# Optimization experiments

Hardware: AMD Instinct MI355X
Metric: run time of the kernel (lower is better)

The kernel has to match this reference:

```python
import jax, jax.numpy as jnp
import numpy as np

B, C1, C2, H, W, NH = 16, 256, 256, 64, 64, 8
C = C2 // 2          # hidden dim of retention blocks (c2*e)
HD = C // NH         # head dim
EPS = 1e-5           # torch BatchNorm2d / LayerNorm default eps


def _ln(x, g, b):
    mu = jnp.mean(x, -1, keepdims=True)
    var = jnp.mean((x - mu) ** 2, -1, keepdims=True)
    return (x - mu) * jax.lax.rsqrt(var + EPS) * g + b


def _bn_silu(y, g, b, m, v):
    # inference-mode BatchNorm2d (running stats) + SiLU, channels axis=1
    y = (y - m[:, None, None]) * jax.lax.rsqrt(v + EPS)[:, None, None] * g[:, None, None] + b[:, None, None]
    return jax.nn.silu(y)


def _decay1d(L, dec):
    # RelPos2d.generate_1d_decay: exp(decay_n * |i-j|), shape (NH, L, L)
    idx = jnp.arange(L)
    m = jnp.abs(idx[:, None] - idx[None, :]).astype(jnp.float32)
    return jnp.exp(dec[:, None, None] * m)


def setup_inputs() -> dict:
    key = jax.random.key(0)
    ks = jax.random.split(key, 8)
    s = 0.02
    return {
        'x': jax.random.normal(ks[0], (B, C1, H, W), jnp.float32),
        'cv1_w': jax.random.normal(ks[1], (2 * C, C1), jnp.float32) * s,
        'bn1_g': jnp.ones((2 * C,)), 'bn1_b': jnp.zeros((2 * C,)),
        'bn1_m': jnp.zeros((2 * C,)), 'bn1_v': jnp.ones((2 * C,)),
        'cv2_w': jax.random.normal(ks[2], (C2, 3 * C), jnp.float32) * s,
        'bn2_g': jnp.ones((C2,)), 'bn2_b': jnp.zeros((C2,)),
        'bn2_m': jnp.zeros((C2,)), 'bn2_v': jnp.ones((C2,)),
        'ln1_g': jnp.ones((C,)), 'ln1_b': jnp.zeros((C,)),
        'qkv_w': jax.random.normal(ks[3], (3 * C, C), jnp.float32) * s,
        'qkv_b': jnp.zeros((3 * C,)),
        'proj_w': jax.random.normal(ks[4], (C, C), jnp.float32) * s,
        'proj_b': jnp.zeros((C,)),
        'gamma': jnp.ones((C,)),
        'ln2_g': jnp.ones((C,)), 'ln2_b': jnp.zeros((C,)),
        'ffn_w1': jax.random.normal(ks[5], (2 * C, C), jnp.float32) * s,
        'ffn_b1': jnp.zeros((2 * C,)),
        'ffn_w2': jax.random.normal(ks[6], (C, 2 * C), jnp.float32) * s,
        'ffn_b2': jnp.zeros((C,)),
    }


def reference(x, cv1_w, bn1_g, bn1_b, bn1_m, bn1_v, cv2_w, bn2_g, bn2_b, bn2_m, bn2_v,
              ln1_g, ln1_b, qkv_w, qkv_b, proj_w, proj_b, gamma,
              ln2_g, ln2_b, ffn_w1, ffn_b1, ffn_w2, ffn_b2):
    # RelPos2d: decay per head, initial_value=2, heads_range=4; mode='chunk' -> 1D decays
    dec = jnp.log(1.0 - 2.0 ** (-2.0 - 4.0 * jnp.arange(NH, dtype=jnp.float32) / NH))
    decay_h = _decay1d(H, dec)  # (NH, H, H)
    decay_w = _decay1d(W, dec)  # (NH, W, W)

    # cv1: 1x1 conv + BN + SiLU, then chunk into two halves of C channels
    y = _bn_silu(jnp.einsum('bchw,oc->bohw', x, cv1_w), bn1_g, bn1_b, bn1_m, bn1_v)
    y1, y2 = y[:, :C], y[:, C:]

    # RetBlock on channels-last feature map
    f = jnp.transpose(y2, (0, 2, 3, 1))  # (B,H,W,C)
    res = f
    fn = _ln(f, ln1_g, ln1_b)
    qkv = fn @ qkv_w.T + qkv_b
    q, k, v = jnp.split(qkv, 3, axis=-1)

    def heads(t):
        return jnp.transpose(t.reshape(B, H, W, NH, HD), (0, 3, 1, 2, 4))  # (B,NH,H,W,HD)

    q, k, v = heads(q), heads(k), heads(v)

    # axial retention: row attention with exponential row-decay
    qk_h = jnp.einsum('bnhwc,bnHwc->bnhHw', q, k) * decay_h[None, :, :, :, None]
    out_h = jnp.einsum('bnhHw,bnHwc->bnhwc', qk_h, v)
    # column attention with exponential column-decay
    qk_w = jnp.einsum('bnhwc,bnhWc->bnhwW', q, k) * decay_w[None, :, None, :, :]
    out_w = jnp.einsum('bnhwW,bnhWc->bnhwc', qk_w, v)
    out = 0.5 * (out_h + out_w)
    out = jnp.transpose(out, (0, 2, 3, 1, 4)).reshape(B, H, W, C)

    f = res + (out @ proj_w.T + proj_b) * gamma
    res2 = f
    fn2 = _ln(f, ln2_g, ln2_b)
    h1 = jax.nn.gelu(fn2 @ ffn_w1.T + ffn_b1, approximate=False)
    f = res2 + (h1 @ ffn_w2.T + ffn_b2)

    f = jnp.transpose(f, (0, 3, 1, 2))  # back to (B,C,H,W)
    cat = jnp.concatenate([y1, y2, f], axis=1)  # (B,3C,H,W)
    return _bn_silu(jnp.einsum('bchw,oc->bohw', cat, cv2_w), bn2_g, bn2_b, bn2_m, bn2_v)
```

## Files before the change

### kernel.cpp

```cpp
#include <hip/hip_runtime.h>
#include <math.h>

#define LEPS 1e-5f
static constexpr int NPOS = 65536;

typedef __attribute__((ext_vector_type(8))) short short8;
typedef __attribute__((ext_vector_type(4))) float floatx4;

__device__ __forceinline__ ushort f2bf(float f) {
    unsigned int u = __float_as_uint(f);
    u += 0x7FFF + ((u >> 16) & 1);
    return (ushort)(u >> 16);
}
__device__ __forceinline__ float bfu(ushort h) {
    return __uint_as_float((unsigned int)h << 16);
}
__device__ __forceinline__ float bfl(unsigned int u) {
    return __uint_as_float(u << 16);
}
__device__ __forceinline__ float bfh(unsigned int u) {
    return __uint_as_float(u & 0xffff0000u);
}

typedef __attribute__((address_space(1))) const unsigned int gu32_t;
typedef __attribute__((address_space(3))) unsigned int lu32_t;
__device__ __forceinline__ void gld16(const ushort* g, ushort* l) {
    __builtin_amdgcn_global_load_lds((gu32_t*)g, (lu32_t*)l, 16, 0, 0);
}

struct WcvtArgs { const float* src[6]; ushort* dst[6]; int n[6]; };
__global__ __launch_bounds__(256)
void wcvt_k(WcvtArgs a)
{
    const int seg = blockIdx.y;
    const float* s = a.src[seg];
    ushort* d = a.dst[seg];
    const int n = a.n[seg];
    for (int i = blockIdx.x * 256 + threadIdx.x; i < n; i += gridDim.x * 256)
        d[i] = f2bf(s[i]);
}

__global__ __launch_bounds__(256)
void bnprep_k(const float* g1, const float* b1, const float* m1, const float* v1,
              const float* g2, const float* b2, const float* m2, const float* v2,
              float* s1, float* h1, float* s2, float* h2)
{
    const int i = threadIdx.x;
    if (blockIdx.x == 0) {
        const float s = g1[i] * rsqrtf(v1[i] + LEPS);
        s1[i] = s; h1[i] = b1[i] - m1[i] * s;
    } else {
        const float s = g2[i] * rsqrtf(v2[i] + LEPS);
        s2[i] = s; h2[i] = b2[i] - m2[i] * s;
    }
}

__global__ __launch_bounds__(256)
void tr_k(const float* __restrict__ x, ushort* __restrict__ xT)
{
    __shared__ float tile[64][65];
    const int t = threadIdx.x;
    const int bi = blockIdx.x;
    const int hwt = bi & 63, ct = (bi >> 6) & 3, b = bi >> 8;
    const int p0 = b * 4096 + hwt * 64, c0 = ct * 64;
    const float* src = x + ((size_t)(b * 256 + c0) << 12) + hwt * 64;
#pragma unroll
    for (int i = 0; i < 16; i++) {
        int cc = (t >> 6) + i * 4;
        tile[cc][t & 63] = src[((size_t)cc << 12) + (t & 63)];
    }
    __syncthreads();
    const int c2 = (t & 31) * 2;
    const int pr = t >> 5;
#pragma unroll
    for (int i = 0; i < 8; i++) {
        int pp = pr + i * 8;
        unsigned int u = (unsigned int)f2bf(tile[c2][pp])
                       | ((unsigned int)f2bf(tile[c2 + 1][pp]) << 16);
        *(unsigned int*)&xT[(size_t)(p0 + pp) * 256 + c0 + c2] = u;
    }
}

template<int KDIM, int ARS, int AMODE, int EPI, int LN>
__global__ __launch_bounds__(256)
void gemm_k(const ushort* __restrict__ A0, const ushort* __restrict__ A1,
            const ushort* __restrict__ Wm, const float* __restrict__ bias,
            const float* __restrict__ q0, const float* __restrict__ q1,
            const ushort* __restrict__ resh,
            const float* __restrict__ lng, const float* __restrict__ lnb,
            ushort* __restrict__ lnout, void* __restrict__ outv, int ors)
{
    constexpr int NT = KDIM / 64;
    __shared__ __align__(16) ushort smem[24576];
    const int t = threadIdx.x;
    const int p0 = blockIdx.x * 64;
    const int o0 = blockIdx.y * 128;
    const int lane = t & 63, wv = t >> 6;
    const int wn = wv * 32;
    const int ln15 = lane & 15, quad = lane >> 4;
    const int dl_row = lane >> 3;
    const int dl_sch = (lane & 7) ^ dl_row;
    const int c_off0 = ((quad) ^ (ln15 & 7)) * 8;
    const int c_off1 = ((4 + quad) ^ (ln15 & 7)) * 8;
    floatx4 acc[4][2] = {};

    const int a3row = t >> 2, a3q = t & 3;
    uint4 ra[2], rb4[2];

    auto stageA = [&](int k0, int bc) {
#pragma unroll
        for (int i = 0; i < 2; i++) {
            const int r0 = wv * 16 + i * 8;
            const int row = r0 + dl_row;
            const ushort* src;
            if (AMODE == 2) {
                if (k0 < 256) src = A0 + (size_t)(p0 + row) * 256 + k0 + dl_sch * 8;
                else          src = A1 + (size_t)(p0 + row) * 128 + (k0 - 256) + dl_sch * 8;
            } else {
                src = A0 + (size_t)(p0 + row) * ARS + k0 + dl_sch * 8;
            }
            gld16(src, &smem[bc * 4096 + r0 * 64]);
        }
    };
    auto stageB = [&](int k0, int bc) {
#pragma unroll
        for (int i = 0; i < 4; i++) {
            const int r0 = wv * 32 + i * 8;
            gld16(Wm + (size_t)(o0 + r0 + dl_row) * KDIM + k0 + dl_sch * 8,
                  &smem[8192 + bc * 8192 + r0 * 64]);
        }
    };
    auto loadA3 = [&](int k0) {
        const ushort* s1 = A0 + (size_t)(p0 + a3row) * 128 + k0 + a3q * 16;
        const ushort* s2 = A1 + (size_t)(p0 + a3row) * 128 + k0 + a3q * 16;
#pragma unroll
        for (int i = 0; i < 2; i++) { ra[i] = ((const uint4*)s1)[i]; rb4[i] = ((const uint4*)s2)[i]; }
    };
    auto writeA3 = [&](int bc) {
#pragma unroll
        for (int i = 0; i < 2; i++) {
            const unsigned int* ap = (const unsigned int*)&ra[i];
            const unsigned int* bp = (const unsigned int*)&rb4[i];
            uint4 w; unsigned int* wp = (unsigned int*)&w;
#pragma unroll
            for (int j = 0; j < 4; j++)
                wp[j] = (unsigned int)f2bf(0.5f * (bfl(ap[j]) + bfl(bp[j])))
                      | ((unsigned int)f2bf(0.5f * (bfh(ap[j]) + bfh(bp[j]))) << 16);
            const int pch = (a3q * 2 + i) ^ (a3row & 7);
            *(uint4*)&smem[bc * 4096 + a3row * 64 + pch * 8] = w;
        }
    };
    auto compute = [&](int bc) {
#pragma unroll
        for (int kh = 0; kh < 2; kh++) {
            const int co = kh ? c_off1 : c_off0;
            short8 a[4], b[2];
#pragma unroll
            for (int i = 0; i < 4; i++)
                a[i] = *(const short8*)&smem[bc * 4096 + (i * 16 + ln15) * 64 + co];
#pragma unroll
            for (int j = 0; j < 2; j++)
                b[j] = *(const short8*)&smem[8192 + bc * 8192 + (wn + j * 16 + ln15) * 64 + co];
#pragma unroll
            for (int i = 0; i < 4; i++)
#pragma unroll
                for (int j = 0; j < 2; j++)
                    acc[i][j] = __builtin_amdgcn_mfma_f32_16x16x32_bf16(
                        a[i], b[j], acc[i][j], 0, 0, 0);
        }
    };

    if (AMODE == 3) {
        loadA3(0);
        stageB(0, 0);
#pragma unroll
        for (int tt = 0; tt < NT; ++tt) {
            const int cur = tt & 1;
            writeA3(cur);
            if (tt + 1 < NT) {
                loadA3((tt + 1) * 64);
                stageB((tt + 1) * 64, cur ^ 1);
                asm volatile("s_waitcnt vmcnt(8) lgkmcnt(0)" ::: "memory");
            } else {
                asm volatile("s_waitcnt vmcnt(0) lgkmcnt(0)" ::: "memory");
            }
            __builtin_amdgcn_s_barrier();
            __builtin_amdgcn_sched_barrier(0);
            compute(cur);
            __builtin_amdgcn_sched_barrier(0);
            __builtin_amdgcn_s_barrier();
        }
    } else {
        stageA(0, 0); stageB(0, 0);
#pragma unroll
        for (int tt = 0; tt < NT; ++tt) {
            const int cur = tt & 1;
            if (tt + 1 < NT) {
                stageA((tt + 1) * 64, cur ^ 1);
                stageB((tt + 1) * 64, cur ^ 1);
                asm volatile("s_waitcnt vmcnt(6)" ::: "memory");
            } else {
                asm volatile("s_waitcnt vmcnt(0)" ::: "memory");
            }
            __builtin_amdgcn_s_barrier();
            __builtin_amdgcn_sched_barrier(0);
            compute(cur);
            __builtin_amdgcn_sched_barrier(0);
            __builtin_amdgcn_s_barrier();
        }
    }

    if (EPI == 2) {
        float* cb = (float*)smem;
        float* ob = (float*)outv + (((size_t)(p0 >> 12) * 256) << 12);
        const int hw0 = p0 & 4095;
#pragma unroll
        for (int chunk = 0; chunk < 2; chunk++) {
            __syncthreads();
            if ((wv >> 1) == chunk) {
#pragma unroll
                for (int i = 0; i < 4; i++)
#pragma unroll
                for (int j = 0; j < 2; j++) {
                    const int chl = (wv & 1) * 32 + j * 16 + ln15;
                    const int o = o0 + chunk * 64 + chl;
                    const float sc = q0[o], sh = q1[o];
#pragma unroll
                    for (int r = 0; r < 4; r++) {
                        const int pos = i * 16 + quad * 4 + r;
                        float v = acc[i][j][r] * sc + sh;
                        v = v / (1.f + __expf(-v));
                        cb[chl * 72 + pos] = v;
                    }
                }
            }
            __syncthreads();
#pragma unroll
            for (int it = 0; it < 4; it++) {
                const int flat = it * 256 + t;
                const int ch = flat >> 4, posq = (flat & 15) * 4;
                const int o = o0 + chunk * 64 + ch;
                float4 v4 = *(const float4*)&cb[ch * 72 + posq];
                *(float4*)&ob[((size_t)o << 12) + hw0 + posq] = v4;
            }
        }
        return;
    }

    const bool lnact = LN && (EPI != 1 || o0 == 128);
    ushort (*lt)[136] = (ushort (*)[136])smem;
#pragma unroll
    for (int i = 0; i < 4; i++) {
#pragma unroll
        for (int r = 0; r < 4; r++) {
            const int lr = i * 16 + quad * 4 + r;
            const int p = p0 + lr;
#pragma unroll
            for (int j = 0; j < 2; j++) {
                const int ol = wn + j * 16 + ln15;
                const int o = o0 + ol;
                float v = acc[i][j][r];
                if (EPI == 0) {
                    v += bias[o];
                } else if (EPI == 1) {
                    v = v * q0[o] + q1[o];
                    v = v / (1.f + __expf(-v));
                } else if (EPI == 4) {
                    v = bfu(resh[(size_t)p * 256 + 128 + o]) + (v + bias[o]) * q0[o];
                }
                lt[lr][ol] = f2bf(v);
            }
        }
    }
    __syncthreads();
    {
        ushort* o16 = (ushort*)outv;
#pragma unroll
        for (int it = 0; it < 4; it++) {
            const int flat = it * 256 + t;
            const int row = flat >> 4, ch = (flat & 15) * 8;
            *(uint4*)&o16[(size_t)(p0 + row) * (size_t)ors + o0 + ch] =
                *(const uint4*)&lt[row][ch];
        }
    }

    if (lnact && t < 128) {
        const int rrow = t >> 1, rhalf = t & 1;
        const ushort* rp = &lt[rrow][rhalf * 64];
        float s = 0.f, s2 = 0.f;
#pragma unroll
        for (int i = 0; i < 8; i++) {
            const uint4 u = *(const uint4*)(rp + i * 8);
            const unsigned int ww[4] = {u.x, u.y, u.z, u.w};
#pragma unroll
            for (int j = 0; j < 4; j++) {
                const float a = bfl(ww[j]), c = bfh(ww[j]);
                s += a + c; s2 += a * a + c * c;
            }
        }
        s += __shfl_xor(s, 1); s2 += __shfl_xor(s2, 1);
        const float mu = s * (1.f / 128.f);
        const float rn = rsqrtf(s2 * (1.f / 128.f) - mu * mu + LEPS);
        ushort* op = lnout + (size_t)(p0 + rrow) * 128 + rhalf * 64;
#pragma unroll
        for (int i = 0; i < 8; i++) {
            const uint4 u = *(const uint4*)(rp + i * 8);
            const unsigned int ww[4] = {u.x, u.y, u.z, u.w};
            uint4 wout;
            unsigned int* wo = (unsigned int*)&wout;
#pragma unroll
            for (int j = 0; j < 4; j++) {
                const int ch = rhalf * 64 + i * 8 + j * 2;
                const float2 gg = *(const float2*)(lng + ch);
                const float2 bb = *(const float2*)(lnb + ch);
                const float a = (bfl(ww[j]) - mu) * rn * gg.x + bb.x;
                const float c = (bfh(ww[j]) - mu) * rn * gg.y + bb.y;
                wo[j] = (unsigned int)f2bf(a) | ((unsigned int)f2bf(c) << 16);
            }
            *(uint4*)(op + i * 8) = wout;
        }
    }
}

__global__ __launch_bounds__(256)
void ffn_k(const ushort* __restrict__ fn2, const ushort* __restrict__ w1,
           const float* __restrict__ b1, const ushort* __restrict__ w2,
           const float* __restrict__ b2, ushort* __restrict__ f)
{
    __shared__ __align__(16) ushort smem[40960];
    const int t = threadIdx.x;
    const int p0 = blockIdx.x * 64;
    const int lane = t & 63, wv = t >> 6;
    const int ln15 = lane & 15, quad = lane >> 4;
    const int dl_row = lane >> 3;
    const int dl_sch = (lane & 7) ^ dl_row;
    const int dl4_row = lane >> 4;
    const int dl4_c   = lane & 15;
    const int c_off0 = ((quad) ^ (ln15 & 7)) * 8;
    const int c_off1 = ((4 + quad) ^ (ln15 & 7)) * 8;

    float bb1[4], bb2[2];
#pragma unroll
    for (int j = 0; j < 4; j++) bb1[j] = b1[wv * 64 + j * 16 + ln15];
#pragma unroll
    for (int j = 0; j < 2; j++) bb2[j] = b2[wv * 32 + j * 16 + ln15];

#pragma unroll
    for (int i = 0; i < 4; i++) {
        const int r0 = wv * 16 + i * 4;
        const int row = r0 + dl4_row;
        const int sch = dl4_c ^ (row & 7);
        gld16(fn2 + (size_t)(p0 + row) * 128 + sch * 8, &smem[r0 * 128]);
    }
#pragma unroll
    for (int i = 0; i < 16; i++) {
        const int r0 = wv * 64 + i * 4;
        const int row = r0 + dl4_row;
        const int sch = dl4_c ^ (row & 7);
        gld16(w1 + (size_t)row * 128 + sch * 8, &smem[8192 + r0 * 128]);
    }
    asm volatile("s_waitcnt vmcnt(0)" ::: "memory");
    __builtin_amdgcn_s_barrier();
    __builtin_amdgcn_sched_barrier(0);

    floatx4 acc1[4][4] = {};
#pragma unroll
    for (int kk = 0; kk < 4; kk++) {
        const int co = ((kk * 4 + quad) ^ (ln15 & 7)) * 8;
        short8 a[4], b[4];
#pragma unroll
        for (int i = 0; i < 4; i++)
            a[i] = *(const short8*)&smem[(i * 16 + ln15) * 128 + co];
#pragma unroll
        for (int j = 0; j < 4; j++)
            b[j] = *(const short8*)&smem[8192 + (wv * 64 + j * 16 + ln15) * 128 + co];
#pragma unroll
        for (int i = 0; i < 4; i++)
#pragma unroll
            for (int j = 0; j < 4; j++)
                acc1[i][j] = __builtin_amdgcn_mfma_f32_16x16x32_bf16(
                    a[i], b[j], acc1[i][j], 0, 0, 0);
    }
    __builtin_amdgcn_s_barrier();
    __builtin_amdgcn_sched_barrier(0);

#pragma unroll
    for (int i = 0; i < 4; i++) {
        const int r0 = wv * 32 + i * 8;
        gld16(w2 + (size_t)(r0 + dl_row) * 256 + dl_sch * 8,
              &smem[16896 + r0 * 64]);
    }
    {
        ushort (*H1w)[264] = (ushort (*)[264])smem;
#pragma unroll
        for (int i = 0; i < 4; i++)
#pragma unroll
        for (int j = 0; j < 4; j++)
#pragma unroll
        for (int r = 0; r < 4; r++) {
            float v = acc1[i][j][r] + bb1[j];
            v = 0.5f * v * (1.f + erff(v * 0.70710678118654752f));
            H1w[i * 16 + quad * 4 + r][wv * 64 + j * 16 + ln15] = f2bf(v);
        }
    }
    asm volatile("s_waitcnt lgkmcnt(0)" ::: "memory");
    __builtin_amdgcn_s_barrier();
    __builtin_amdgcn_sched_barrier(0);

    ushort (*H1)[264] = (ushort (*)[264])smem;
    floatx4 acc2[4][2] = {};
#pragma unroll
    for (int t4 = 0; t4 < 4; ++t4) {
        const int cur = t4 & 1;
        if (t4 + 1 < 4) {
#pragma unroll
            for (int i = 0; i < 4; i++) {
                const int r0 = wv * 32 + i * 8;
                gld16(w2 + (size_t)(r0 + dl_row) * 256 + (t4 + 1) * 64 + dl_sch * 8,
                      &smem[16896 + (cur ^ 1) * 8192 + r0 * 64]);
            }
            asm volatile("s_waitcnt vmcnt(4)" ::: "memory");
        } else {
#pragma unroll
            for (int i = 0; i < 4; i++) {
                const int r0 = wv * 16 + i * 4;
                gld16(f + (size_t)(p0 + r0 + (lane >> 4)) * 128 + (lane & 15) * 8,
                      &smem[16896 + (cur ^ 1) * 8192 + r0 * 128]);
            }
            asm volatile("s_waitcnt vmcnt(4)" ::: "memory");
        }
        __builtin_amdgcn_s_barrier();
        __builtin_amdgcn_sched_barrier(0);
#pragma unroll
        for (int kh = 0; kh < 2; kh++) {
            const int co = kh ? c_off1 : c_off0;
            short8 a[4], b[2];
#pragma unroll
            for (int i = 0; i < 4; i++)
                a[i] = *(const short8*)&H1[i * 16 + ln15][t4 * 64 + kh * 32 + quad * 8];
#pragma unroll
            for (int j = 0; j < 2; j++)
                b[j] = *(const short8*)&smem[16896 + cur * 8192
                                             + (wv * 32 + j * 16 + ln15) * 64 + co];
#pragma unroll
            for (int i = 0; i < 4; i++)
#pragma unroll
                for (int j = 0; j < 2; j++)
                    acc2[i][j] = __builtin_amdgcn_mfma_f32_16x16x32_bf16(
                        a[i], b[j], acc2[i][j], 0, 0, 0);
        }
        __builtin_amdgcn_sched_barrier(0);
        __builtin_amdgcn_s_barrier();
    }
    asm volatile("s_waitcnt vmcnt(0)" ::: "memory");
    __builtin_amdgcn_s_barrier();

    ushort* Ft = &smem[16896];
    {
#pragma unroll
        for (int i = 0; i < 4; i++)
#pragma unroll
        for (int r = 0; r < 4; r++) {
            const int pos = i * 16 + quad * 4 + r;
#pragma unroll
            for (int j = 0; j < 2; j++) {
                const int ch = wv * 32 + j * 16 + ln15;
                const int idx = pos * 128 + ch;
                Ft[idx] = f2bf(bfu(Ft[idx]) + acc2[i][j][r] + bb2[j]);
            }
        }
    }
    __syncthreads();
#pragma unroll
    for (int it = 0; it < 4; it++) {
        const int flat = it * 256 + t;
        const int row = flat >> 4, ch = (flat & 15) * 8;
        *(uint4*)&f[(size_t)(p0 + row) * 128 + ch] = *(const uint4*)&Ft[row * 128 + ch];
    }
}

__global__ __launch_bounds__(256)
void attn_k(const ushort* __restrict__ qkv, ushort* __restrict__ oh,
            ushort* __restrict__ ow)
{
    __shared__ ushort VtS[4][16 * 72];
    __shared__ ushort SbS[4][64 * 72];
    __shared__ float dpow[128];
    const int t = threadIdx.x, wv = t >> 6, lane = t & 63;
    const int ln15 = lane & 15, quad = lane >> 4;
    const int dirH = (blockIdx.y == 0);
    ushort* outb = dirH ? oh : ow;
    const int blk = blockIdx.x;
    const int lg = blk & 15, n = (blk >> 4) & 7, b = blk >> 7;
    if (t < 128) {
        const float dec = logf(1.f - exp2f(-2.f - 0.5f * (float)n));
        int d = t - 63; if (d < 0) d = -d;
        dpow[t] = __expf(dec * (float)d);
    }
    const int fixed = lg * 4 + wv;
    const int stride = dirH ? 64 : 1;
    const size_t base = (size_t)b * 4096 + (dirH ? fixed : fixed * 64);
    const size_t cbase = base * 384 + n * 16;

    {
        const ushort* vp = qkv + cbase + (size_t)lane * stride * 384 + 256;
        const uint4 va = *(const uint4*)vp, vb = *(const uint4*)(vp + 8);
        ushort* vt = VtS[wv] + lane;
        const unsigned int w[8] = { va.x, va.y, va.z, va.w, vb.x, vb.y, vb.z, vb.w };
#pragma unroll
        for (int d = 0; d < 8; d++) {
            vt[(2 * d) * 72]     = (ushort)(w[d] & 0xffff);
            vt[(2 * d + 1) * 72] = (ushort)(w[d] >> 16);
        }
    }
    short8 qa[4], kb[4];
    {
        const short8 z = {0, 0, 0, 0, 0, 0, 0, 0};
#pragma unroll
        for (int mt = 0; mt < 4; mt++) {
            const int i = mt * 16 + ln15;
            if (quad < 2) {
                const ushort* qp = qkv + cbase + (size_t)i * stride * 384 + quad * 8;
                qa[mt] = *(const short8*)qp;
                kb[mt] = *(const short8*)(qp + 128);
            } else { qa[mt] = z; kb[mt] = z; }
        }
    }
    __syncthreads();

#pragma unroll
    for (int mt = 0; mt < 4; mt++) {
#pragma unroll
        for (int nt = 0; nt < 4; nt++) {
            floatx4 c = {0.f, 0.f, 0.f, 0.f};
            c = __builtin_amdgcn_mfma_f32_16x16x32_bf16(qa[mt], kb[nt], c, 0, 0, 0);
            const int i0 = mt * 16 + quad * 4;
            const int jl = nt * 16 + ln15;
            const float* lut = dpow + (i0 - jl + 63);
            ushort* sb = SbS[wv] + i0 * 72 + jl;
#pragma unroll
            for (int r = 0; r < 4; r++)
                sb[r * 72] = f2bf(c[r] * lut[r]);
        }
    }
    __syncthreads();

    short8 av[2];
#pragma unroll
    for (int c = 0; c < 2; c++)
        av[c] = *(const short8*)&VtS[wv][ln15 * 72 + c * 32 + quad * 8];
    floatx4 o[4] = {};
#pragma unroll
    for (int nt4 = 0; nt4 < 4; nt4++) {
#pragma unroll
        for (int c = 0; c < 2; c++) {
            const short8 bs = *(const short8*)
                &SbS[wv][(nt4 * 16 + ln15) * 72 + c * 32 + quad * 8];
            o[nt4] = __builtin_amdgcn_mfma_f32_16x16x32_bf16(av[c], bs, o[nt4], 0, 0, 0);
        }
    }
#pragma unroll
    for (int nt4 = 0; nt4 < 4; nt4++) {
        const int i = nt4 * 16 + ln15;
        ushort* op = outb + (base + (size_t)i * stride) * 128 + n * 16 + quad * 4;
        uint2 w;
        w.x = (unsigned int)f2bf(o[nt4][0]) | ((unsigned int)f2bf(o[nt4][1]) << 16);
        w.y = (unsigned int)f2bf(o[nt4][2]) | ((unsigned int)f2bf(o[nt4][3]) << 16);
        *(uint2*)op = w;
    }
}

extern "C" void kernel_launch(void* const* d_in, const int* in_sizes, int n_in,
                              void* d_out, int out_size, void* d_ws, size_t ws_size,
                              hipStream_t stream)
{
    const float* x      = (const float*)d_in[0];
    const float* cv1_w  = (const float*)d_in[1];
    const float* bn1_g  = (const float*)d_in[2];
    const float* bn1_b  = (const float*)d_in[3];
    const float* bn1_m  = (const float*)d_in[4];
    const float* bn1_v  = (const float*)d_in[5];
    const float* cv2_w  = (const float*)d_in[6];
    const float* bn2_g  = (const float*)d_in[7];
    const float* bn2_b  = (const float*)d_in[8];
    const float* bn2_m  = (const float*)d_in[9];
    const float* bn2_v  = (const float*)d_in[10];
    const float* ln1_g  = (const float*)d_in[11];
    const float* ln1_b  = (const float*)d_in[12];
    const float* qkv_w  = (const float*)d_in[13];
    const float* qkv_b  = (const float*)d_in[14];
    const float* proj_w = (const float*)d_in[15];
    const float* proj_b = (const float*)d_in[16];
    const float* gamma  = (const float*)d_in[17];
    const float* ln2_g  = (const float*)d_in[18];
    const float* ln2_b  = (const float*)d_in[19];
    const float* ffn_w1 = (const float*)d_in[20];
    const float* ffn_b1 = (const float*)d_in[21];
    const float* ffn_w2 = (const float*)d_in[22];
    const float* ffn_b2 = (const float*)d_in[23];

    ushort* W = (ushort*)d_ws;
    ushort* y    = W;
    ushort* f    = y    + (size_t)NPOS * 256;
    ushort* tmp  = f    + (size_t)NPOS * 128;
    ushort* owb  = tmp  + (size_t)NPOS * 128;
    ushort* qkvb = owb  + (size_t)NPOS * 128;
    ushort* xT   = qkvb + (size_t)NPOS * 384;
    ushort* wc1  = xT   + (size_t)NPOS * 256;
    ushort* wqkv = wc1  + 65536;
    ushort* wpr  = wqkv + 49152;
    ushort* ww1  = wpr  + 16384;
    ushort* ww2  = ww1  + 32768;
    ushort* wc2  = ww2  + 32768;
    float*  bns1 = (float*)(wc2 + 98304);
    float*  bnb1 = bns1 + 256;
    float*  bns2 = bnb1 + 256;
    float*  bnb2 = bns2 + 256;
    float*  out  = (float*)d_out;

    WcvtArgs wa;
    wa.src[0] = cv1_w;  wa.dst[0] = wc1;  wa.n[0] = 65536;
    wa.src[1] = qkv_w;  wa.dst[1] = wqkv; wa.n[1] = 49152;
    wa.src[2] = proj_w; wa.dst[2] = wpr;  wa.n[2] = 16384;
    wa.src[3] = ffn_w1; wa.dst[3] = ww1;  wa.n[3] = 32768;
    wa.src[4] = ffn_w2; wa.dst[4] = ww2;  wa.n[4] = 32768;
    wa.src[5] = cv2_w;  wa.dst[5] = wc2;  wa.n[5] = 98304;
    wcvt_k<<<dim3(96, 6), 256, 0, stream>>>(wa);
    bnprep_k<<<2, 256, 0, stream>>>(bn1_g, bn1_b, bn1_m, bn1_v,
                                    bn2_g, bn2_b, bn2_m, bn2_v,
                                    bns1, bnb1, bns2, bnb2);
    tr_k<<<4096, 256, 0, stream>>>(x, xT);

    gemm_k<256, 256, 0, 1, 1><<<dim3(1024, 2), 256, 0, stream>>>(
        xT, nullptr, wc1, nullptr, bns1, bnb1, nullptr, ln1_g, ln1_b, tmp, y, 256);
    gemm_k<128, 128, 0, 0, 0><<<dim3(1024, 3), 256, 0, stream>>>(
        tmp, nullptr, wqkv, qkv_b, nullptr, nullptr, nullptr, nullptr, nullptr,
        nullptr, qkvb, 384);
    attn_k<<<dim3(2048, 2), 256, 0, stream>>>(qkvb, tmp, owb);
    gemm_k<128, 128, 3, 4, 1><<<dim3(1024, 1), 256, 0, stream>>>(
        tmp, owb, wpr, proj_b, gamma, nullptr, y, ln2_g, ln2_b, tmp, f, 128);
    ffn_k<<<1024, 256, 0, stream>>>(tmp, ww1, ffn_b1, ww2, ffn_b2, f);
    gemm_k<384, 0, 2, 2, 0><<<dim3(1024, 2), 256, 0, stream>>>(
        y, f, wc2, nullptr, bns2, bnb2, nullptr, nullptr, nullptr, nullptr, out, 0);
}
```

Measured before the change: 334.2 us.

## Fuse projection, residual, LayerNorm2 and FFN into one kernel

Merges the proj GEMM (with the out_h/out_w averaging, bias, gamma and residual) and the FFN kernel into a single pf_k kernel. The post-projection residual stays in registers and LayerNorm2 is computed in shared memory, so the f and fn2 intermediates no longer round-trip through global memory, and one launch is removed. To fit shared memory, the FFN first GEMM is restructured to stream w1 in 64-row chunks. This may reduce overlap or occupancy compared with the previous two-kernel arrangement.

```diff
diff --git a/kernel.cpp b/kernel.cpp
--- a/kernel.cpp
+++ b/kernel.cpp
@@ -86,7 +86,6 @@
 void gemm_k(const ushort* __restrict__ A0, const ushort* __restrict__ A1,
             const ushort* __restrict__ Wm, const float* __restrict__ bias,
             const float* __restrict__ q0, const float* __restrict__ q1,
-            const ushort* __restrict__ resh,
             const float* __restrict__ lng, const float* __restrict__ lnb,
             ushort* __restrict__ lnout, void* __restrict__ outv, int ors)
 {
@@ -104,9 +103,6 @@
     const int c_off1 = ((4 + quad) ^ (ln15 & 7)) * 8;
     floatx4 acc[4][2] = {};
 
-    const int a3row = t >> 2, a3q = t & 3;
-    uint4 ra[2], rb4[2];
-
     auto stageA = [&](int k0, int bc) {
 #pragma unroll
         for (int i = 0; i < 2; i++) {
@@ -130,26 +126,6 @@
                   &smem[8192 + bc * 8192 + r0 * 64]);
         }
     };
-    auto loadA3 = [&](int k0) {
-        const ushort* s1 = A0 + (size_t)(p0 + a3row) * 128 + k0 + a3q * 16;
-        const ushort* s2 = A1 + (size_t)(p0 + a3row) * 128 + k0 + a3q * 16;
-#pragma unroll
-        for (int i = 0; i < 2; i++) { ra[i] = ((const uint4*)s1)[i]; rb4[i] = ((const uint4*)s2)[i]; }
-    };
-    auto writeA3 = [&](int bc) {
-#pragma unroll
-        for (int i = 0; i < 2; i++) {
-            const unsigned int* ap = (const unsigned int*)&ra[i];
-            const unsigned int* bp = (const unsigned int*)&rb4[i];
-            uint4 w; unsigned int* wp = (unsigned int*)&w;
-#pragma unroll
-            for (int j = 0; j < 4; j++)
-                wp[j] = (unsigned int)f2bf(0.5f * (bfl(ap[j]) + bfl(bp[j])))
-                      | ((unsigned int)f2bf(0.5f * (bfh(ap[j]) + bfh(bp[j]))) << 16);
-            const int pch = (a3q * 2 + i) ^ (a3row & 7);
-            *(uint4*)&smem[bc * 4096 + a3row * 64 + pch * 8] = w;
-        }
-    };
     auto compute = [&](int bc) {
 #pragma unroll
         for (int kh = 0; kh < 2; kh++) {
@@ -170,44 +146,22 @@
         }
     };
 
-    if (AMODE == 3) {
-        loadA3(0);
-        stageB(0, 0);
-#pragma unroll
-        for (int tt = 0; tt < NT; ++tt) {
-            const int cur = tt & 1;
-            writeA3(cur);
-            if (tt + 1 < NT) {
-                loadA3((tt + 1) * 64);
-                stageB((tt + 1) * 64, cur ^ 1);
-                asm volatile("s_waitcnt vmcnt(8) lgkmcnt(0)" ::: "memory");
-            } else {
-                asm volatile("s_waitcnt vmcnt(0) lgkmcnt(0)" ::: "memory");
-            }
-            __builtin_amdgcn_s_barrier();
-            __builtin_amdgcn_sched_barrier(0);
-            compute(cur);
-            __builtin_amdgcn_sched_barrier(0);
-            __builtin_amdgcn_s_barrier();
-        }
-    } else {
-        stageA(0, 0); stageB(0, 0);
-#pragma unroll
-        for (int tt = 0; tt < NT; ++tt) {
-            const int cur = tt & 1;
-            if (tt + 1 < NT) {
-                stageA((tt + 1) * 64, cur ^ 1);
-                stageB((tt + 1) * 64, cur ^ 1);
-                asm volatile("s_waitcnt vmcnt(6)" ::: "memory");
-            } else {
-                asm volatile("s_waitcnt vmcnt(0)" ::: "memory");
-            }
-            __builtin_amdgcn_s_barrier();
-            __builtin_amdgcn_sched_barrier(0);
-            compute(cur);
-            __builtin_amdgcn_sched_barrier(0);
-            __builtin_amdgcn_s_barrier();
-        }
+    stageA(0, 0); stageB(0, 0);
+#pragma unroll
+    for (int tt = 0; tt < NT; ++tt) {
+        const int cur = tt & 1;
+        if (tt + 1 < NT) {
+            stageA((tt + 1) * 64, cur ^ 1);
+            stageB((tt + 1) * 64, cur ^ 1);
+            asm volatile("s_waitcnt vmcnt(6)" ::: "memory");
+        } else {
+            asm volatile("s_waitcnt vmcnt(0)" ::: "memory");
+        }
+        __builtin_amdgcn_s_barrier();
+        __builtin_amdgcn_sched_barrier(0);
+        compute(cur);
+        __builtin_amdgcn_sched_barrier(0);
+        __builtin_amdgcn_s_barrier();
     }
 
     if (EPI == 2) {
@@ -254,7 +208,6 @@
 #pragma unroll
         for (int r = 0; r < 4; r++) {
             const int lr = i * 16 + quad * 4 + r;
-            const int p = p0 + lr;
 #pragma unroll
             for (int j = 0; j < 2; j++) {
                 const int ol = wn + j * 16 + ln15;
@@ -262,11 +215,9 @@
                 float v = acc[i][j][r];
                 if (EPI == 0) {
                     v += bias[o];
-                } else if (EPI == 1) {
+                } else {
                     v = v * q0[o] + q1[o];
                     v = v / (1.f + __expf(-v));
-                } else if (EPI == 4) {
-                    v = bfu(resh[(size_t)p * 256 + 128 + o]) + (v + bias[o]) * q0[o];
                 }
                 lt[lr][ol] = f2bf(v);
             }
@@ -323,15 +274,20 @@
 }
 
 __global__ __launch_bounds__(256)
-void ffn_k(const ushort* __restrict__ fn2, const ushort* __restrict__ w1,
-           const float* __restrict__ b1, const ushort* __restrict__ w2,
-           const float* __restrict__ b2, ushort* __restrict__ f)
+void pf_k(const ushort* __restrict__ oh, const ushort* __restrict__ ow,
+          const ushort* __restrict__ wpr, const float* __restrict__ pb,
+          const float* __restrict__ gamma, const ushort* __restrict__ resh,
+          const float* __restrict__ lng, const float* __restrict__ lnb,
+          const ushort* __restrict__ w1, const float* __restrict__ b1,
+          const ushort* __restrict__ w2, const float* __restrict__ b2,
+          ushort* __restrict__ f)
 {
-    __shared__ __align__(16) ushort smem[40960];
+    __shared__ __align__(16) ushort smem[33280];
     const int t = threadIdx.x;
     const int p0 = blockIdx.x * 64;
     const int lane = t & 63, wv = t >> 6;
     const int ln15 = lane & 15, quad = lane >> 4;
+    const int wn = wv * 32;
     const int dl_row = lane >> 3;
     const int dl_sch = (lane & 7) ^ dl_row;
     const int dl4_row = lane >> 4;
@@ -339,95 +295,201 @@
     const int c_off0 = ((quad) ^ (ln15 & 7)) * 8;
     const int c_off1 = ((4 + quad) ^ (ln15 & 7)) * 8;
 
-    float bb1[4], bb2[2];
-#pragma unroll
-    for (int j = 0; j < 4; j++) bb1[j] = b1[wv * 64 + j * 16 + ln15];
-#pragma unroll
-    for (int j = 0; j < 2; j++) bb2[j] = b2[wv * 32 + j * 16 + ln15];
-
+    const int a3row = t >> 2, a3q = t & 3;
+    uint4 ra[2], rb4[2];
+    auto loadA3 = [&](int k0) {
+        const ushort* s1 = oh + (size_t)(p0 + a3row) * 128 + k0 + a3q * 16;
+        const ushort* s2 = ow + (size_t)(p0 + a3row) * 128 + k0 + a3q * 16;
+#pragma unroll
+        for (int i = 0; i < 2; i++) { ra[i] = ((const uint4*)s1)[i]; rb4[i] = ((const uint4*)s2)[i]; }
+    };
+    auto writeA3 = [&](int bc) {
+#pragma unroll
+        for (int i = 0; i < 2; i++) {
+            const unsigned int* ap = (const unsigned int*)&ra[i];
+            const unsigned int* bp = (const unsigned int*)&rb4[i];
+            uint4 w; unsigned int* wp = (unsigned int*)&w;
+#pragma unroll
+            for (int j = 0; j < 4; j++)
+                wp[j] = (unsigned int)f2bf(0.5f * (bfl(ap[j]) + bfl(bp[j])))
+                      | ((unsigned int)f2bf(0.5f * (bfh(ap[j]) + bfh(bp[j]))) << 16);
+            const int pch = (a3q * 2 + i) ^ (a3row & 7);
+            *(uint4*)&smem[bc * 4096 + a3row * 64 + pch * 8] = w;
+        }
+    };
+    floatx4 accP[4][2] = {};
+
+    loadA3(0);
+#pragma unroll
+    for (int i = 0; i < 8; i++) {
+        const int r0 = wv * 32 + i * 4;
+        const int row = r0 + dl4_row;
+        gld16(wpr + (size_t)row * 128 + (dl4_c ^ (row & 7)) * 8,
+              &smem[8192 + r0 * 128]);
+    }
+#pragma unroll
+    for (int tt = 0; tt < 2; ++tt) {
+        const int cur = tt & 1;
+        writeA3(cur);
+        if (tt == 0) {
+            loadA3(64);
+            asm volatile("s_waitcnt vmcnt(8) lgkmcnt(0)" ::: "memory");
+        } else {
+            asm volatile("s_waitcnt vmcnt(0) lgkmcnt(0)" ::: "memory");
+        }
+        __builtin_amdgcn_s_barrier();
+        __builtin_amdgcn_sched_barrier(0);
+#pragma unroll
+        for (int kh = 0; kh < 2; kh++) {
+            const int coA = kh ? c_off1 : c_off0;
+            const int coB = ((tt * 8 + kh * 4 + quad) ^ (ln15 & 7)) * 8;
+            short8 a[4], b[2];
+#pragma unroll
+            for (int i = 0; i < 4; i++)
+                a[i] = *(const short8*)&smem[cur * 4096 + (i * 16 + ln15) * 64 + coA];
+#pragma unroll
+            for (int j = 0; j < 2; j++)
+                b[j] = *(const short8*)&smem[8192 + (wn + j * 16 + ln15) * 128 + coB];
+#pragma unroll
+            for (int i = 0; i < 4; i++)
+#pragma unroll
+                for (int j = 0; j < 2; j++)
+                    accP[i][j] = __builtin_amdgcn_mfma_f32_16x16x32_bf16(
+                        a[i], b[j], accP[i][j], 0, 0, 0);
+        }
+        __builtin_amdgcn_sched_barrier(0);
+        __builtin_amdgcn_s_barrier();
+    }
+
+    float fp[4][2][4];
+    ushort (*lt)[136] = (ushort (*)[136])&smem[8192];
+#pragma unroll
+    for (int i = 0; i < 4; i++)
+#pragma unroll
+    for (int r = 0; r < 4; r++) {
+        const int lr = i * 16 + quad * 4 + r;
+        const int p = p0 + lr;
+#pragma unroll
+        for (int j = 0; j < 2; j++) {
+            const int o = wn + j * 16 + ln15;
+            float v = bfu(resh[(size_t)p * 256 + 128 + o]) + (accP[i][j][r] + pb[o]) * gamma[o];
+            fp[i][j][r] = v;
+            lt[lr][o] = f2bf(v);
+        }
+    }
 #pragma unroll
     for (int i = 0; i < 4; i++) {
         const int r0 = wv * 16 + i * 4;
         const int row = r0 + dl4_row;
-        const int sch = dl4_c ^ (row & 7);
-        gld16(fn2 + (size_t)(p0 + row) * 128 + sch * 8, &smem[r0 * 128]);
-    }
-#pragma unroll
-    for (int i = 0; i < 16; i++) {
-        const int r0 = wv * 64 + i * 4;
-        const int row = r0 + dl4_row;
-        const int sch = dl4_c ^ (row & 7);
-        gld16(w1 + (size_t)row * 128 + sch * 8, &smem[8192 + r0 * 128]);
-    }
-    asm volatile("s_waitcnt vmcnt(0)" ::: "memory");
-    __builtin_amdgcn_s_barrier();
-    __builtin_amdgcn_sched_barrier(0);
-
-    floatx4 acc1[4][4] = {};
-#pragma unroll
-    for (int kk = 0; kk < 4; kk++) {
-        const int co = ((kk * 4 + quad) ^ (ln15 & 7)) * 8;
-        short8 a[4], b[4];
-#pragma unroll
-        for (int i = 0; i < 4; i++)
-            a[i] = *(const short8*)&smem[(i * 16 + ln15) * 128 + co];
-#pragma unroll
-        for (int j = 0; j < 4; j++)
-            b[j] = *(const short8*)&smem[8192 + (wv * 64 + j * 16 + ln15) * 128 + co];
-#pragma unroll
-        for (int i = 0; i < 4; i++)
-#pragma unroll
-            for (int j = 0; j < 4; j++)
-                acc1[i][j] = __builtin_amdgcn_mfma_f32_16x16x32_bf16(
-                    a[i], b[j], acc1[i][j], 0, 0, 0);
-    }
-    __builtin_amdgcn_s_barrier();
-    __builtin_amdgcn_sched_barrier(0);
-
-#pragma unroll
-    for (int i = 0; i < 4; i++) {
-        const int r0 = wv * 32 + i * 8;
-        gld16(w2 + (size_t)(r0 + dl_row) * 256 + dl_sch * 8,
-              &smem[16896 + r0 * 64]);
-    }
-    {
-        ushort (*H1w)[264] = (ushort (*)[264])smem;
-#pragma unroll
-        for (int i = 0; i < 4; i++)
-#pragma unroll
-        for (int j = 0; j < 4; j++)
-#pragma unroll
-        for (int r = 0; r < 4; r++) {
-            float v = acc1[i][j][r] + bb1[j];
-            v = 0.5f * v * (1.f + erff(v * 0.70710678118654752f));
-            H1w[i * 16 + quad * 4 + r][wv * 64 + j * 16 + ln15] = f2bf(v);
+        gld16(w1 + (size_t)row * 128 + (dl4_c ^ (row & 7)) * 8,
+              &smem[25088 + r0 * 128]);
+    }
+    __syncthreads();
+    if (t < 128) {
+        const int rrow = t >> 1, rhalf = t & 1;
+        const ushort* rp = &lt[rrow][rhalf * 64];
+        float s = 0.f, s2 = 0.f;
+#pragma unroll
+        for (int i = 0; i < 8; i++) {
+            const uint4 u = *(const uint4*)(rp + i * 8);
+            const unsigned int ww[4] = {u.x, u.y, u.z, u.w};
+#pragma unroll
+            for (int j = 0; j < 4; j++) {
+                const float a = bfl(ww[j]), c = bfh(ww[j]);
+                s += a + c; s2 += a * a + c * c;
+            }
+        }
+        s += __shfl_xor(s, 1); s2 += __shfl_xor(s2, 1);
+        const float mu = s * (1.f / 128.f);
+        const float rn = rsqrtf(s2 * (1.f / 128.f) - mu * mu + LEPS);
+#pragma unroll
+        for (int i = 0; i < 8; i++) {
+            const uint4 u = *(const uint4*)(rp + i * 8);
+            const unsigned int ww[4] = {u.x, u.y, u.z, u.w};
+            uint4 wout;
+            unsigned int* wo = (unsigned int*)&wout;
+#pragma unroll
+            for (int j = 0; j < 4; j++) {
+                const int ch = rhalf * 64 + i * 8 + j * 2;
+                const float2 gg = *(const float2*)(lng + ch);
+                const float2 bb = *(const float2*)(lnb + ch);
+                const float a = (bfl(ww[j]) - mu) * rn * gg.x + bb.x;
+                const float c = (bfh(ww[j]) - mu) * rn * gg.y + bb.y;
+                wo[j] = (unsigned int)f2bf(a) | ((unsigned int)f2bf(c) << 16);
+            }
+            const int c16 = (rhalf * 8 + i) ^ (rrow & 7);
+            *(uint4*)&smem[rrow * 128 + c16 * 8] = wout;
         }
     }
     asm volatile("s_waitcnt lgkmcnt(0)" ::: "memory");
     __builtin_amdgcn_s_barrier();
     __builtin_amdgcn_sched_barrier(0);
 
-    ushort (*H1)[264] = (ushort (*)[264])smem;
+    ushort* H1 = &smem[8192];
+    float bb2[2];
+#pragma unroll
+    for (int j = 0; j < 2; j++) bb2[j] = b2[wn + j * 16 + ln15];
+#pragma unroll
+    for (int q = 0; q < 4; q++) {
+        asm volatile("s_waitcnt vmcnt(0)" ::: "memory");
+        __builtin_amdgcn_s_barrier();
+        __builtin_amdgcn_sched_barrier(0);
+        const float bq = b1[q * 64 + wv * 16 + ln15];
+        floatx4 a1[4] = {};
+#pragma unroll
+        for (int kk = 0; kk < 4; kk++) {
+            const int co = ((kk * 4 + quad) ^ (ln15 & 7)) * 8;
+            short8 bfr = *(const short8*)&smem[25088 + (wv * 16 + ln15) * 128 + co];
+#pragma unroll
+            for (int i = 0; i < 4; i++) {
+                short8 afr = *(const short8*)&smem[(i * 16 + ln15) * 128 + co];
+                a1[i] = __builtin_amdgcn_mfma_f32_16x16x32_bf16(afr, bfr, a1[i], 0, 0, 0);
+            }
+        }
+#pragma unroll
+        for (int i = 0; i < 4; i++)
+#pragma unroll
+        for (int r = 0; r < 4; r++) {
+            float v = a1[i][r] + bq;
+            v = 0.5f * v * (1.f + erff(v * 0.70710678118654752f));
+            H1[(i * 16 + quad * 4 + r) * 264 + q * 64 + wv * 16 + ln15] = f2bf(v);
+        }
+        __builtin_amdgcn_sched_barrier(0);
+        __builtin_amdgcn_s_barrier();
+        if (q < 3) {
+#pragma unroll
+            for (int i = 0; i < 4; i++) {
+                const int r0 = wv * 16 + i * 4;
+                const int row = r0 + dl4_row;
+                gld16(w1 + (size_t)((q + 1) * 64 + row) * 128 + (dl4_c ^ (row & 7)) * 8,
+                      &smem[25088 + r0 * 128]);
+            }
+        }
+    }
+#pragma unroll
+    for (int i = 0; i < 4; i++) {
+        const int r0 = wv * 32 + i * 8;
+        gld16(w2 + (size_t)(r0 + dl_row) * 256 + dl_sch * 8, &smem[25088 + r0 * 64]);
+    }
+    asm volatile("s_waitcnt lgkmcnt(0)" ::: "memory");
+    __builtin_amdgcn_s_barrier();
+    __builtin_amdgcn_sched_barrier(0);
+
     floatx4 acc2[4][2] = {};
 #pragma unroll
     for (int t4 = 0; t4 < 4; ++t4) {
-        const int cur = t4 & 1;
+        const int curb = (t4 & 1) ? 0 : 25088;
+        const int nxtb = (t4 & 1) ? 25088 : 0;
         if (t4 + 1 < 4) {
 #pragma unroll
             for (int i = 0; i < 4; i++) {
                 const int r0 = wv * 32 + i * 8;
                 gld16(w2 + (size_t)(r0 + dl_row) * 256 + (t4 + 1) * 64 + dl_sch * 8,
-                      &smem[16896 + (cur ^ 1) * 8192 + r0 * 64]);
+                      &smem[nxtb + r0 * 64]);
             }
             asm volatile("s_waitcnt vmcnt(4)" ::: "memory");
         } else {
-#pragma unroll
-            for (int i = 0; i < 4; i++) {
-                const int r0 = wv * 16 + i * 4;
-                gld16(f + (size_t)(p0 + r0 + (lane >> 4)) * 128 + (lane & 15) * 8,
-                      &smem[16896 + (cur ^ 1) * 8192 + r0 * 128]);
-            }
-            asm volatile("s_waitcnt vmcnt(4)" ::: "memory");
+            asm volatile("s_waitcnt vmcnt(0)" ::: "memory");
         }
         __builtin_amdgcn_s_barrier();
         __builtin_amdgcn_sched_barrier(0);
@@ -437,11 +499,10 @@
             short8 a[4], b[2];
 #pragma unroll
             for (int i = 0; i < 4; i++)
-                a[i] = *(const short8*)&H1[i * 16 + ln15][t4 * 64 + kh * 32 + quad * 8];
+                a[i] = *(const short8*)&H1[(i * 16 + ln15) * 264 + t4 * 64 + kh * 32 + quad * 8];
 #pragma unroll
             for (int j = 0; j < 2; j++)
-                b[j] = *(const short8*)&smem[16896 + cur * 8192
-                                             + (wv * 32 + j * 16 + ln15) * 64 + co];
+                b[j] = *(const short8*)&smem[curb + (wn + j * 16 + ln15) * 64 + co];
 #pragma unroll
             for (int i = 0; i < 4; i++)
 #pragma unroll
@@ -452,30 +513,23 @@
         __builtin_amdgcn_sched_barrier(0);
         __builtin_amdgcn_s_barrier();
     }
-    asm volatile("s_waitcnt vmcnt(0)" ::: "memory");
-    __builtin_amdgcn_s_barrier();
-
-    ushort* Ft = &smem[16896];
-    {
-#pragma unroll
-        for (int i = 0; i < 4; i++)
-#pragma unroll
-        for (int r = 0; r < 4; r++) {
-            const int pos = i * 16 + quad * 4 + r;
-#pragma unroll
-            for (int j = 0; j < 2; j++) {
-                const int ch = wv * 32 + j * 16 + ln15;
-                const int idx = pos * 128 + ch;
-                Ft[idx] = f2bf(bfu(Ft[idx]) + acc2[i][j][r] + bb2[j]);
-            }
-        }
+
+    ushort (*lt2)[136] = (ushort (*)[136])&smem[8192];
+#pragma unroll
+    for (int i = 0; i < 4; i++)
+#pragma unroll
+    for (int r = 0; r < 4; r++) {
+        const int lr = i * 16 + quad * 4 + r;
+#pragma unroll
+        for (int j = 0; j < 2; j++)
+            lt2[lr][wn + j * 16 + ln15] = f2bf(fp[i][j][r] + acc2[i][j][r] + bb2[j]);
     }
     __syncthreads();
 #pragma unroll
     for (int it = 0; it < 4; it++) {
         const int flat = it * 256 + t;
         const int row = flat >> 4, ch = (flat & 15) * 8;
-        *(uint4*)&f[(size_t)(p0 + row) * 128 + ch] = *(const uint4*)&Ft[row * 128 + ch];
+        *(uint4*)&f[(size_t)(p0 + row) * 128 + ch] = *(const uint4*)&lt2[row][ch];
     }
 }
 
@@ -632,14 +686,13 @@
     tr_k<<<4096, 256, 0, stream>>>(x, xT);
 
     gemm_k<256, 256, 0, 1, 1><<<dim3(1024, 2), 256, 0, stream>>>(
-        xT, nullptr, wc1, nullptr, bns1, bnb1, nullptr, ln1_g, ln1_b, tmp, y, 256);
+        xT, nullptr, wc1, nullptr, bns1, bnb1, ln1_g, ln1_b, tmp, y, 256);
     gemm_k<128, 128, 0, 0, 0><<<dim3(1024, 3), 256, 0, stream>>>(
-        tmp, nullptr, wqkv, qkv_b, nullptr, nullptr, nullptr, nullptr, nullptr,
+        tmp, nullptr, wqkv, qkv_b, nullptr, nullptr, nullptr, nullptr,
         nullptr, qkvb, 384);
     attn_k<<<dim3(2048, 2), 256, 0, stream>>>(qkvb, tmp, owb);
-    gemm_k<128, 128, 3, 4, 1><<<dim3(1024, 1), 256, 0, stream>>>(
-        tmp, owb, wpr, proj_b, gamma, nullptr, y, ln2_g, ln2_b, tmp, f, 128);
-    ffn_k<<<1024, 256, 0, stream>>>(tmp, ww1, ffn_b1, ww2, ffn_b2, f);
+    pf_k<<<1024, 256, 0, stream>>>(
+        tmp, owb, wpr, proj_b, gamma, y, ln2_g, ln2_b, ww1, ffn_b1, ww2, ffn_b2, f);
     gemm_k<384, 0, 2, 2, 0><<<dim3(1024, 2), 256, 0, stream>>>(
-        y, f, wc2, nullptr, bns2, bnb2, nullptr, nullptr, nullptr, nullptr, out, 0);
-}
+        y, f, wc2, nullptr, bns2, bnb2, nullptr, nullptr, nullptr, out, 0);
+}
```

Measured after the change: 378.2 us. 1.13x slower.
